# Kernel optimization log

Measured on AMD Instinct MI355X. Metric: run time of the kernel, lower is better.

The kernel has to match this reference:

```python
import jax, jax.numpy as jnp
import numpy as np

B, S, H = 2, 2048, 2048
NH, NKV, HD = 16, 8, 128
EPS = 1e-6
THETA = 10000.0
SCALE = HD ** -0.5


def setup_inputs() -> dict:
    key = jax.random.key(0)
    ks = jax.random.split(key, 6)
    return {
        "positions": jnp.tile(jnp.arange(S, dtype=jnp.int64 if jax.config.jax_enable_x64 else jnp.int32), (B, 1)),
        "hidden_states": jax.random.normal(ks[0], (B, S, H), jnp.float32),
        "residual": jax.random.normal(ks[1], (B, S, H), jnp.float32),
        "layernorm_weight": 1.0 + 0.02 * jax.random.normal(ks[2], (H,), jnp.float32),
        "qkv_weight": 0.02 * jax.random.normal(ks[3], ((NH + 2 * NKV) * HD, H), jnp.float32),
        "o_weight": 0.02 * jax.random.normal(ks[4], (H, NH * HD), jnp.float32),
        "q_norm_weight": 1.0 + 0.02 * jax.random.normal(ks[5], (HD,), jnp.float32),
        "k_norm_weight": jnp.ones((HD,), jnp.float32),
    }


def _rmsnorm(x, w, eps=EPS):
    return x * jax.lax.rsqrt(jnp.mean(x * x, axis=-1, keepdims=True) + eps) * w


def _rope(x, positions):
    # x: [B, S, h, HD]; neox-style rotate-half RoPE
    inv_freq = 1.0 / (THETA ** (jnp.arange(0, HD, 2, dtype=jnp.float32) / HD))
    ang = positions.astype(jnp.float32)[..., None] * inv_freq  # [B, S, HD/2]
    cos = jnp.cos(ang)[:, :, None, :]
    sin = jnp.sin(ang)[:, :, None, :]
    x1, x2 = jnp.split(x, 2, axis=-1)
    return jnp.concatenate([x1 * cos - x2 * sin, x2 * cos + x1 * sin], axis=-1)


def reference(positions, hidden_states, residual, layernorm_weight,
              qkv_weight, o_weight, q_norm_weight, k_norm_weight):
    # Fused RMSNorm + QKV projection (on unnormalized hidden_states)
    xn = _rmsnorm(hidden_states, layernorm_weight)
    qkv = jnp.einsum('bsh,oh->bso', xn, qkv_weight)  # [B, S, (NH+2*NKV)*HD]
    q, k, v = jnp.split(qkv, [NH * HD, (NH + NKV) * HD], axis=-1)
    q = q.reshape(B, S, NH, HD)
    k = k.reshape(B, S, NKV, HD)
    v = v.reshape(B, S, NKV, HD)
    # per-head q/k RMSNorm (q_norm in fused QKV kernel, k_norm inside attention)
    q = _rmsnorm(q, q_norm_weight)
    k = _rmsnorm(k, k_norm_weight)
    # RoPE
    q = _rope(q, positions)
    k = _rope(k, positions)
    # GQA: expand KV heads
    rep = NH // NKV
    k = jnp.repeat(k, rep, axis=2)
    v = jnp.repeat(v, rep, axis=2)
    # causal attention
    scores = jnp.einsum('bqhd,bkhd->bhqk', q, k) * SCALE
    causal = jnp.tril(jnp.ones((S, S), bool))
    scores = jnp.where(causal[None, None], scores, jnp.finfo(scores.dtype).min)
    probs = jax.nn.softmax(scores, axis=-1)
    attn = jnp.einsum('bhqk,bkhd->bqhd', probs, v).reshape(B, S, NH * HD)
    # fused output projection + residual add
    return jnp.einsum('bsd,hd->bsh', attn, o_weight) + residual
```

## Files before the change

### kernel.cpp

```cpp
#include <hip/hip_runtime.h>
#include <hip/hip_bf16.h>

typedef __attribute__((ext_vector_type(8))) short bf16x8;
typedef __attribute__((ext_vector_type(4))) float f32x4;

#define B_ 2
#define S_ 2048
#define H_ 2048
#define NH_ 16
#define NKV_ 8
#define HD_ 128
#define M_ (B_ * S_)
#define NQKV_ ((NH_ + 2 * NKV_) * HD_)
#define QK_SCALE 0.08838834764831845f

#define VMCNT(n) asm volatile("s_waitcnt vmcnt(" #n ")" ::: "memory")

__device__ __forceinline__ unsigned short f2bf(float f) {
  unsigned int u = __float_as_uint(f);
  u += 0x7fffu + ((u >> 16) & 1u);
  return (unsigned short)(u >> 16);
}
__device__ __forceinline__ float bf2f(unsigned short h) {
  return __uint_as_float(((unsigned int)h) << 16);
}
__device__ __forceinline__ void gload_lds16(const void* g, void* l) {
  __builtin_amdgcn_global_load_lds(
      (const __attribute__((address_space(1))) void*)g,
      (__attribute__((address_space(3))) void*)l, 16, 0, 0);
}

__global__ __launch_bounds__(256) void k_rmsnorm(
    const float* __restrict__ x, const float* __restrict__ w,
    unsigned short* __restrict__ out) {
  __shared__ float red[4];
  const int m = blockIdx.x;
  const int t = threadIdx.x;
  const float4* row = (const float4*)(x + (size_t)m * H_);
  float4 v0 = row[t];
  float4 v1 = row[t + 256];
  float ss = v0.x * v0.x + v0.y * v0.y + v0.z * v0.z + v0.w * v0.w +
             v1.x * v1.x + v1.y * v1.y + v1.z * v1.z + v1.w * v1.w;
#pragma unroll
  for (int mk = 1; mk < 64; mk <<= 1) ss += __shfl_xor(ss, mk);
  if ((t & 63) == 0) red[t >> 6] = ss;
  __syncthreads();
  ss = red[0] + red[1] + red[2] + red[3];
  const float sc = rsqrtf(ss * (1.0f / H_) + 1e-6f);
  const float4* wv = (const float4*)w;
  float4 w0 = wv[t], w1 = wv[t + 256];
  ushort4 o0, o1;
  o0.x = f2bf(v0.x * sc * w0.x);
  o0.y = f2bf(v0.y * sc * w0.y);
  o0.z = f2bf(v0.z * sc * w0.z);
  o0.w = f2bf(v0.w * sc * w0.w);
  o1.x = f2bf(v1.x * sc * w1.x);
  o1.y = f2bf(v1.y * sc * w1.y);
  o1.z = f2bf(v1.z * sc * w1.z);
  o1.w = f2bf(v1.w * sc * w1.w);
  ushort4* orow = (ushort4*)(out + (size_t)m * H_);
  orow[t] = o0;
  orow[t + 256] = o1;
}

__global__ __launch_bounds__(256) void k_f32_to_bf16(
    const float* __restrict__ in, unsigned short* __restrict__ out, int n4) {
  int idx = blockIdx.x * 256 + threadIdx.x;
  const int stride = gridDim.x * 256;
  for (; idx < n4; idx += stride) {
    float4 v = ((const float4*)in)[idx];
    ushort4 o;
    o.x = f2bf(v.x);
    o.y = f2bf(v.y);
    o.z = f2bf(v.z);
    o.w = f2bf(v.w);
    ((ushort4*)out)[idx] = o;
  }
}

__global__ __launch_bounds__(256) void k_rope_table(
    const int* __restrict__ positions, float* __restrict__ cos_t,
    float* __restrict__ sin_t) {
  int idx = blockIdx.x * 256 + threadIdx.x;
  if (idx >= B_ * S_ * 64) return;
  int d = idx & 63;
  int bs = idx >> 6;
  float pos = (float)positions[bs];
  float inv_freq = powf(10000.0f, -(float)(2 * d) * (1.0f / HD_));
  float ang = pos * inv_freq;
  cos_t[idx] = cosf(ang);
  sin_t[idx] = sinf(ang);
}

template <int FMB>
__device__ __forceinline__ void load_a256(const unsigned short* sAb, int wm,
                                          int lr, int lg, bf16x8 (&af)[2][4]) {
#pragma unroll
  for (int kk = 0; kk < 2; ++kk) {
    const int pc = kk * 4 + lg;
#pragma unroll
    for (int i = 0; i < 4; ++i) {
      const int R = wm + (FMB + i) * 16 + lr;
      const int idx = ((R >> 6) & 1) * 8192 +
                      ((((R >> 7) << 6) | (R & 63)) << 6) +
                      ((pc ^ (R & 7)) << 3);
      af[kk][i] = *(const bf16x8*)&sAb[idx];
    }
  }
}
template <int FNB>
__device__ __forceinline__ void load_b256(const unsigned short* sBb, int wn,
                                          int lr, int lg, bf16x8 (&bfv)[2][2]) {
#pragma unroll
  for (int kk = 0; kk < 2; ++kk) {
    const int pc = kk * 4 + lg;
#pragma unroll
    for (int j = 0; j < 2; ++j) {
      const int R = wn + (FNB + j) * 16 + lr;
      const int idx = ((R >> 5) & 1) * 8192 +
                      ((((R >> 6) << 5) | (R & 31)) << 6) +
                      ((pc ^ (R & 7)) << 3);
      bfv[kk][j] = *(const bf16x8*)&sBb[idx];
    }
  }
}

template <int FMB, int FNB>
__device__ __forceinline__ void phase_mfma(const bf16x8 (&af)[2][4],
                                           const bf16x8 (&bfv)[2][2],
                                           f32x4 (&acc)[8][4]) {
#pragma unroll
  for (int kk = 0; kk < 2; ++kk)
#pragma unroll
    for (int i = 0; i < 4; ++i)
#pragma unroll
      for (int j = 0; j < 2; ++j)
        acc[FMB + i][FNB + j] = __builtin_amdgcn_mfma_f32_16x16x32_bf16(
            af[kk][i], bfv[kk][j], acc[FMB + i][FNB + j], 0, 0, 0);
}

__global__ __launch_bounds__(512, 2) void k_gemm256(
    const unsigned short* __restrict__ A, const unsigned short* __restrict__ Bt,
    unsigned short* __restrict__ C, int M, int N, int K) {
  __shared__ unsigned short sA[2][256 * 64];
  __shared__ unsigned short sB[2][256 * 64];
  const int tid = threadIdx.x;
  const int w = tid >> 6;
  const int l = tid & 63;
  const int lr = l & 15, lg = l >> 4;
  const int gx = gridDim.x;
  const int lin = blockIdx.y * gx + blockIdx.x;
  const int cpx = (gx * gridDim.y) >> 3;
  const int swz = (lin & 7) * cpx + (lin >> 3);
  const int m0 = (swz / gx) * 256, n0 = (swz % gx) * 256;
  const int wm = (w >> 2) * 128, wn = (w & 3) * 64;
  f32x4 acc[8][4] = {};

  auto stageA = [&](int t, int bufi, int h) {
    const int k0 = t * 64;
#pragma unroll
    for (int i = 0; i < 2; ++i) {
      const int L = i * 512 + tid;
      const int r = L >> 3;
      const int R = ((r >> 6) << 7) | (h << 6) | (r & 63);
      const int d = (L & 7) ^ (r & 7);
      gload_lds16(A + (size_t)(m0 + R) * K + k0 + d * 8,
                  (char*)sA[bufi] + h * 16384 +
                      (size_t)(i * 512 + w * 64) * 16);
    }
  };
  auto stageB = [&](int t, int bufi, int h) {
    const int k0 = t * 64;
#pragma unroll
    for (int i = 0; i < 2; ++i) {
      const int L = i * 512 + tid;
      const int r = L >> 3;
      const int R = ((r >> 5) << 6) | (h << 5) | (r & 31);
      const int d = (L & 7) ^ (r & 7);
      gload_lds16(Bt + (size_t)(n0 + R) * K + k0 + d * 8,
                  (char*)sB[bufi] + h * 16384 +
                      (size_t)(i * 512 + w * 64) * 16);
    }
  };

#define BARR()                          \
  __builtin_amdgcn_s_barrier();         \
  __builtin_amdgcn_sched_barrier(0)
#define LGKM0()                                        \
  asm volatile("s_waitcnt lgkmcnt(0)" ::: "memory");   \
  __builtin_amdgcn_sched_barrier(0)

  stageA(0, 0, 0);
  stageB(0, 0, 0);
  stageB(0, 0, 1);
  stageA(0, 0, 1);
  VMCNT(2);
  BARR();

  bf16x8 af[2][4];
  bf16x8 bfv0[2][2];
  bf16x8 bfv1[2][2];
  const int NT = K >> 6;
  for (int t = 0; t < NT; ++t) {
    const int bufi = t & 1;
    const int nb = bufi ^ 1;
    const bool st = (t + 1 < NT);
    load_a256<0>(sA[bufi], wm, lr, lg, af);
    load_b256<0>(sB[bufi], wn, lr, lg, bfv0);
    load_b256<2>(sB[bufi], wn, lr, lg, bfv1);
    if (st) {
      stageA(t + 1, nb, 0);
      stageB(t + 1, nb, 0);
    }
    __builtin_amdgcn_s_barrier();
    LGKM0();
    __builtin_amdgcn_s_setprio(1);
    phase_mfma<0, 0>(af, bfv0, acc);
    phase_mfma<0, 2>(af, bfv1, acc);
    __builtin_amdgcn_s_setprio(0);
    if (st) {
      VMCNT(4);
    } else {
      VMCNT(0);
    }
    BARR();
    load_a256<4>(sA[bufi], wm, lr, lg, af);
    if (st) {
      stageB(t + 1, nb, 1);
      stageA(t + 1, nb, 1);
    }
    __builtin_amdgcn_s_barrier();
    LGKM0();
    __builtin_amdgcn_s_setprio(1);
    phase_mfma<4, 2>(af, bfv1, acc);
    phase_mfma<4, 0>(af, bfv0, acc);
    __builtin_amdgcn_s_setprio(0);
    if (st) VMCNT(2);
    BARR();
  }

#pragma unroll
  for (int fm = 0; fm < 8; ++fm)
#pragma unroll
    for (int fn = 0; fn < 4; ++fn)
#pragma unroll
      for (int r = 0; r < 4; ++r) {
        const int row = m0 + wm + fm * 16 + lg * 4 + r;
        const int col = n0 + wn + fn * 16 + lr;
        C[(size_t)row * N + col] = f2bf(acc[fm][fn][r]);
      }
#undef BARR
#undef LGKM0
}

template <int FMB>
__device__ __forceinline__ void load_ao(const unsigned short* sAb, int wm,
                                        int lr, int lg, bf16x8 (&af)[2][2]) {
#pragma unroll
  for (int kk = 0; kk < 2; ++kk) {
    const int pc = kk * 4 + lg;
#pragma unroll
    for (int i = 0; i < 2; ++i) {
      const int R = wm + (FMB + i) * 16 + lr;
      const int idx = ((R >> 5) & 1) * 8192 +
                      ((((R >> 6) << 5) | (R & 31)) << 6) +
                      ((pc ^ (R & 7)) << 3);
      af[kk][i] = *(const bf16x8*)&sAb[idx];
    }
  }
}
template <int FNB>
__device__ __forceinline__ void load_bo(const unsigned short* sBb, int wn,
                                        int lr, int lg, bf16x8 (&bfv)[2][2]) {
#pragma unroll
  for (int kk = 0; kk < 2; ++kk) {
    const int pc = kk * 4 + lg;
#pragma unroll
    for (int j = 0; j < 2; ++j) {
      const int R = wn + (FNB + j) * 16 + lr;
      const int idx = ((R >> 5) & 1) * 4096 +
                      ((((R >> 6) << 5) | (R & 31)) << 6) +
                      ((pc ^ (R & 7)) << 3);
      bfv[kk][j] = *(const bf16x8*)&sBb[idx];
    }
  }
}

template <int FMB, int FNB>
__device__ __forceinline__ void phase_mfma_o(const bf16x8 (&af)[2][2],
                                             const bf16x8 (&bfv)[2][2],
                                             f32x4 (&acc)[4][4]) {
#pragma unroll
  for (int kk = 0; kk < 2; ++kk)
#pragma unroll
    for (int i = 0; i < 2; ++i)
#pragma unroll
      for (int j = 0; j < 2; ++j)
        acc[FMB + i][FNB + j] = __builtin_amdgcn_mfma_f32_16x16x32_bf16(
            af[kk][i], bfv[kk][j], acc[FMB + i][FNB + j], 0, 0, 0);
}

__global__ __launch_bounds__(512, 1) void k_gemm_ores(
    const unsigned short* __restrict__ A, const unsigned short* __restrict__ Bt,
    float* __restrict__ Cout, const float* __restrict__ resid, int M, int N,
    int K) {
  __shared__ unsigned short sA[2][256 * 64];
  __shared__ unsigned short sB[2][128 * 64];
  const int tid = threadIdx.x;
  const int w = tid >> 6;
  const int l = tid & 63;
  const int lr = l & 15, lg = l >> 4;
  const int gx = gridDim.x;
  const int lin = blockIdx.y * gx + blockIdx.x;
  const int cpx = (gx * gridDim.y) >> 3;
  const int swz = (lin & 7) * cpx + (lin >> 3);
  const int m0 = (swz / gx) * 256, n0 = (swz % gx) * 128;
  const int wm = (w >> 1) * 64, wn = (w & 1) * 64;
  f32x4 acc[4][4] = {};

  auto stageAo = [&](int t, int bufi, int h) {
    const int k0 = t * 64;
#pragma unroll
    for (int i = 0; i < 2; ++i) {
      const int L = i * 512 + tid;
      const int r = L >> 3;
      const int R = ((r >> 5) << 6) | (h << 5) | (r & 31);
      const int d = (L & 7) ^ (r & 7);
      gload_lds16(A + (size_t)(m0 + R) * K + k0 + d * 8,
                  (char*)sA[bufi] + h * 16384 +
                      (size_t)(i * 512 + w * 64) * 16);
    }
  };
  auto stageBo = [&](int t, int bufi, int h) {
    const int k0 = t * 64;
    const int L = tid;
    const int r = L >> 3;
    const int R = ((r >> 5) << 6) | (h << 5) | (r & 31);
    const int d = (L & 7) ^ (r & 7);
    gload_lds16(Bt + (size_t)(n0 + R) * K + k0 + d * 8,
                (char*)sB[bufi] + h * 8192 + (size_t)(w * 64) * 16);
  };

#define BARR()                          \
  __builtin_amdgcn_s_barrier();         \
  __builtin_amdgcn_sched_barrier(0)
#define LGKM0()                                        \
  asm volatile("s_waitcnt lgkmcnt(0)" ::: "memory");   \
  __builtin_amdgcn_sched_barrier(0)

  stageAo(0, 0, 0);
  stageBo(0, 0, 0);
  stageBo(0, 0, 1);
  stageAo(0, 0, 1);
  VMCNT(2);
  BARR();

  bf16x8 af[2][2];
  bf16x8 bfv0[2][2];
  bf16x8 bfv1[2][2];
  const int NT = K >> 6;
  for (int t = 0; t < NT; ++t) {
    const int bufi = t & 1;
    const int nb = bufi ^ 1;
    const bool st = (t + 1 < NT);
    load_ao<0>(sA[bufi], wm, lr, lg, af);
    load_bo<0>(sB[bufi], wn, lr, lg, bfv0);
    load_bo<2>(sB[bufi], wn, lr, lg, bfv1);
    if (st) {
      stageAo(t + 1, nb, 0);
      stageBo(t + 1, nb, 0);
    }
    __builtin_amdgcn_s_barrier();
    LGKM0();
    __builtin_amdgcn_s_setprio(1);
    phase_mfma_o<0, 0>(af, bfv0, acc);
    phase_mfma_o<0, 2>(af, bfv1, acc);
    __builtin_amdgcn_s_setprio(0);
    if (st) {
      VMCNT(3);
    } else {
      VMCNT(0);
    }
    BARR();
    load_ao<2>(sA[bufi], wm, lr, lg, af);
    if (st) {
      stageBo(t + 1, nb, 1);
      stageAo(t + 1, nb, 1);
    }
    __builtin_amdgcn_s_barrier();
    LGKM0();
    __builtin_amdgcn_s_setprio(1);
    phase_mfma_o<2, 2>(af, bfv1, acc);
    phase_mfma_o<2, 0>(af, bfv0, acc);
    __builtin_amdgcn_s_setprio(0);
    if (st) VMCNT(2);
    BARR();
  }

#pragma unroll
  for (int i = 0; i < 4; ++i)
#pragma unroll
    for (int j = 0; j < 4; ++j)
#pragma unroll
      for (int r = 0; r < 4; ++r) {
        const int row = m0 + wm + i * 16 + lg * 4 + r;
        const int col = n0 + wn + j * 16 + lr;
        const size_t o = (size_t)row * N + col;
        Cout[o] = acc[i][j][r] + resid[o];
      }
#undef BARR
#undef LGKM0
}

__global__ __launch_bounds__(256) void k_postprocess(
    const unsigned short* __restrict__ qkv, const float* __restrict__ qw,
    const float* __restrict__ kw, const float* __restrict__ cos_t,
    const float* __restrict__ sin_t, unsigned short* __restrict__ qb,
    unsigned short* __restrict__ kb, unsigned short* __restrict__ vb) {
  const int m = blockIdx.x;
  const int b = m >> 11, s = m & (S_ - 1);
  const int w = threadIdx.x >> 6, l = threadIdx.x & 63;
  const unsigned short* row = qkv + (size_t)m * NQKV_;
  const float c = cos_t[(size_t)m * 64 + l];
  const float sn = sin_t[(size_t)m * 64 + l];
  for (int hh = w * 8; hh < w * 8 + 8; ++hh) {
    int base, type;
    unsigned short* out;
    const float* nw;
    if (hh < NH_) {
      type = 0;
      base = hh * HD_;
      out = qb + ((size_t)(b * NH_ + hh) * S_ + s) * HD_;
      nw = qw;
    } else if (hh < NH_ + NKV_) {
      int kh = hh - NH_;
      type = 1;
      base = NH_ * HD_ + kh * HD_;
      out = kb + ((size_t)(b * NKV_ + kh) * S_ + s) * HD_;
      nw = kw;
    } else {
      int kh = hh - NH_ - NKV_;
      type = 2;
      base = (NH_ + NKV_) * HD_ + kh * HD_;
      out = vb + ((size_t)(b * NKV_ + kh) * S_ + s) * HD_;
      nw = nullptr;
    }
    unsigned short r1 = row[base + l];
    unsigned short r2 = row[base + 64 + l];
    if (type == 2) {
      out[l] = r1;
      out[64 + l] = r2;
      continue;
    }
    float x1 = bf2f(r1), x2 = bf2f(r2);
    float ss = x1 * x1 + x2 * x2;
#pragma unroll
    for (int mk = 1; mk < 64; mk <<= 1) ss += __shfl_xor(ss, mk);
    float sc = rsqrtf(ss * (1.0f / HD_) + 1e-6f);
    float y1 = x1 * sc * nw[l];
    float y2 = x2 * sc * nw[64 + l];
    float o1 = y1 * c - y2 * sn;
    float o2 = y2 * c + y1 * sn;
    if (type == 0) {
      o1 *= QK_SCALE;
      o2 *= QK_SCALE;
    }
    out[l] = f2bf(o1);
    out[64 + l] = f2bf(o2);
  }
}

__global__ __launch_bounds__(256) void k_transpose_v(
    const unsigned short* __restrict__ in,
    unsigned short* __restrict__ out) {
  __shared__ unsigned short tile[32][33];
  const int bx = blockIdx.x, by = blockIdx.y, bz = blockIdx.z;
  const unsigned short* src = in + (size_t)bz * S_ * HD_;
  unsigned short* dst = out + (size_t)bz * S_ * HD_;
  const int tx = threadIdx.x & 31, ty = threadIdx.x >> 5;
#pragma unroll
  for (int i = ty; i < 32; i += 8)
    tile[i][tx] = src[(size_t)(bx * 32 + i) * HD_ + by * 32 + tx];
  __syncthreads();
#pragma unroll
  for (int i = ty; i < 32; i += 8)
    dst[(size_t)(by * 32 + i) * S_ + bx * 32 + tx] = tile[tx][i];
}

#define MFIX 13.0f
__global__ __launch_bounds__(512, 4) void k_attn(
    const unsigned short* __restrict__ Q,
    const unsigned short* __restrict__ K,
    const unsigned short* __restrict__ VT,
    unsigned short* __restrict__ Oa) {
  __shared__ unsigned short kt[2][64 * 128];
  __shared__ unsigned short vt[2][128 * 64];
  __shared__ unsigned short pls[8 * 16 * 64];
  const int bh = blockIdx.y;
  const int b = bh >> 4, h = bh & 15;
  const int kvh = b * NKV_ + (h >> 1);
  const int xa = blockIdx.x;
  const int xb = 31 - xa;
  const int tid = threadIdx.x;
  const int w = tid >> 6, l = tid & 63;
  const int lr = l & 15, lg = l >> 4;
  const int wr = (w & 3) * 16;
  const int myx = (w < 4) ? xa : xb;
  const int q0m = myx * 64;

  bf16x8 qf[4];
  {
    const unsigned short* Qp = Q + ((size_t)bh * S_ + q0m + wr) * HD_;
#pragma unroll
    for (int tt = 0; tt < 4; ++tt)
      qf[tt] = *(const bf16x8*)(Qp + (size_t)lr * HD_ + tt * 32 + lg * 8);
  }
  f32x4 ao[8] = {};
  float lsum = 0.f;
  const unsigned short* Kp = K + (size_t)kvh * S_ * HD_;
  const unsigned short* Vp = VT + (size_t)kvh * HD_ * S_;
  unsigned short* pw = pls + w * 1024;
  const int psw = (lr & 7) << 1;

  auto stage = [&](int t, int bufi) {
    const int k0 = t * 64;
#pragma unroll
    for (int i = 0; i < 2; ++i) {
      const int chunk = i * 512 + tid;
      {
        const int r = chunk >> 4, p = chunk & 15;
        const int d = p ^ (r & 7);
        gload_lds16(Kp + (size_t)(k0 + r) * HD_ + d * 8,
                    (char*)kt[bufi] + (size_t)(i * 512 + w * 64) * 16);
      }
      {
        const int r = chunk >> 3, p = chunk & 7;
        const int d = p ^ (r & 7);
        gload_lds16(Vp + (size_t)r * S_ + k0 + d * 8,
                    (char*)vt[bufi] + (size_t)(i * 512 + w * 64) * 16);
      }
    }
  };

  auto process = [&](int t, int bufi, bool diag) {
    const unsigned short* ktb = kt[bufi];
    const unsigned short* vtb = vt[bufi];
    f32x4 sc[4] = {};
    __builtin_amdgcn_s_setprio(1);
#pragma unroll
    for (int j = 0; j < 4; ++j)
#pragma unroll
      for (int tt = 0; tt < 4; ++tt) {
        bf16x8 kf = *(const bf16x8*)&ktb[(j * 16 + lr) * 128 +
                                         (((tt * 4 + lg) ^ (lr & 7)) << 3)];
        sc[j] =
            __builtin_amdgcn_mfma_f32_16x16x32_bf16(kf, qf[tt], sc[j], 0, 0, 0);
      }
    __builtin_amdgcn_s_setprio(0);
    if (diag) {
      const int qg = q0m + wr + lr;
      const int kvb = t * 64 + lg * 4;
#pragma unroll
      for (int j = 0; j < 4; ++j)
#pragma unroll
        for (int r = 0; r < 4; ++r)
          if (kvb + j * 16 + r > qg) sc[j][r] = -1e30f;
    }
#pragma unroll
    for (int j = 0; j < 4; ++j) {
      float p0 = __expf(sc[j][0] - MFIX);
      float p1 = __expf(sc[j][1] - MFIX);
      float p2 = __expf(sc[j][2] - MFIX);
      float p3 = __expf(sc[j][3] - MFIX);
      lsum += (p0 + p1) + (p2 + p3);
      unsigned int d0 = (unsigned int)f2bf(p0) | ((unsigned int)f2bf(p1) << 16);
      unsigned int d1 = (unsigned int)f2bf(p2) | ((unsigned int)f2bf(p3) << 16);
      const int g = (4 * j + lg) ^ psw;
      uint2 v;
      v.x = d0;
      v.y = d1;
      *(uint2*)&pw[lr * 64 + g * 4] = v;
    }
    __builtin_amdgcn_s_setprio(1);
#pragma unroll
    for (int ks = 0; ks < 2; ++ks) {
      const int g0 = (8 * ks + 2 * lg) ^ psw;
      bf16x8 pf = *(const bf16x8*)&pw[lr * 64 + g0 * 4];
#pragma unroll
      for (int dj = 0; dj < 8; ++dj) {
        bf16x8 vf = *(const bf16x8*)&vtb[(dj * 16 + lr) * 64 +
                                         (((ks * 4 + lg) ^ (lr & 7)) << 3)];
        ao[dj] =
            __builtin_amdgcn_mfma_f32_16x16x32_bf16(vf, pf, ao[dj], 0, 0, 0);
      }
    }
    __builtin_amdgcn_s_setprio(0);
  };

  stage(0, 0);
  __syncthreads();
  int cur = 0;
  for (int t = 0; t <= xb; ++t) {
    if (t < xb) stage(t + 1, cur ^ 1);
    if (t <= myx) process(t, cur, t == myx);
    __syncthreads();
    cur ^= 1;
  }

  lsum += __shfl_xor(lsum, 16);
  lsum += __shfl_xor(lsum, 32);
  const float inv = 1.0f / lsum;
  const int sg = q0m + wr + lr;
  unsigned short* orow = Oa + ((size_t)b * S_ + sg) * (NH_ * HD_) + h * HD_;
#pragma unroll
  for (int dj = 0; dj < 8; ++dj) {
    ushort4 ov;
    ov.x = f2bf(ao[dj][0] * inv);
    ov.y = f2bf(ao[dj][1] * inv);
    ov.z = f2bf(ao[dj][2] * inv);
    ov.w = f2bf(ao[dj][3] * inv);
    *(ushort4*)&orow[dj * 16 + lg * 4] = ov;
  }
}

extern "C" void kernel_launch(void* const* d_in, const int* in_sizes, int n_in,
                              void* d_out, int out_size, void* d_ws,
                              size_t ws_size, hipStream_t stream) {
  const int* positions = (const int*)d_in[0];
  const float* hidden = (const float*)d_in[1];
  const float* residual = (const float*)d_in[2];
  const float* ln_w = (const float*)d_in[3];
  const float* qkv_w = (const float*)d_in[4];
  const float* o_w = (const float*)d_in[5];
  const float* q_nw = (const float*)d_in[6];
  const float* k_nw = (const float*)d_in[7];

  char* ws = (char*)d_ws;
  const size_t SZ_XN = (size_t)M_ * H_ * 2;
  const size_t SZ_QKVW = (size_t)NQKV_ * H_ * 2;
  const size_t SZ_OW = (size_t)H_ * (NH_ * HD_) * 2;
  const size_t SZ_QKV = (size_t)M_ * NQKV_ * 2;
  const size_t SZ_KB = (size_t)B_ * NKV_ * S_ * HD_ * 2;
  const size_t SZ_COS = (size_t)B_ * S_ * 64 * 4;

  unsigned short* xn = (unsigned short*)(ws);
  unsigned short* q_buf = (unsigned short*)(ws);
  unsigned short* qkvw_bf = (unsigned short*)(ws + SZ_XN);
  unsigned short* k_buf = (unsigned short*)(ws + SZ_XN);
  unsigned short* v_buf = (unsigned short*)(ws + SZ_XN + SZ_KB);
  unsigned short* owbf = (unsigned short*)(ws + SZ_XN + SZ_QKVW);
  unsigned short* qkv_bf = (unsigned short*)(ws + SZ_XN + SZ_QKVW + SZ_OW);
  unsigned short* attn_o = qkv_bf;
  unsigned short* vt_buf =
      (unsigned short*)(ws + SZ_XN + SZ_QKVW + SZ_OW + SZ_QKV);
  float* cos_t = (float*)(ws + SZ_XN + SZ_QKVW + SZ_OW + SZ_QKV + SZ_KB);
  float* sin_t = (float*)((char*)cos_t + SZ_COS);

  k_rmsnorm<<<M_, 256, 0, stream>>>(hidden, ln_w, xn);
  k_f32_to_bf16<<<2048, 256, 0, stream>>>(qkv_w, qkvw_bf,
                                          (int)(SZ_QKVW / 2 / 4));
  k_f32_to_bf16<<<1024, 256, 0, stream>>>(o_w, owbf, (int)(SZ_OW / 2 / 4));
  k_rope_table<<<(B_ * S_ * 64) / 256, 256, 0, stream>>>(positions, cos_t,
                                                         sin_t);
  k_gemm256<<<dim3(NQKV_ / 256, M_ / 256), 512, 0, stream>>>(
      xn, qkvw_bf, qkv_bf, M_, NQKV_, H_);
  k_postprocess<<<M_, 256, 0, stream>>>(qkv_bf, q_nw, k_nw, cos_t, sin_t,
                                        q_buf, k_buf, v_buf);
  k_transpose_v<<<dim3(S_ / 32, HD_ / 32, B_ * NKV_), 256, 0, stream>>>(v_buf,
                                                                        vt_buf);
  k_attn<<<dim3(16, B_ * NH_), 512, 0, stream>>>(q_buf, k_buf, vt_buf, attn_o);
  k_gemm_ores<<<dim3((NH_ * HD_) / 128, M_ / 256), 512, 0, stream>>>(
      attn_o, owbf, (float*)d_out, residual, M_, NH_ * HD_, H_);
}
```

Baseline: 222.4 us.

## Rebalance causal attention work by splitting late KV tiles between wave groups

In the paired-tile causal attention kernel, group A waves used to finish their short query tile early and then idle while group B processed the long tile. Now group A writes its output early, reloads Q for tile B, and takes half of each remaining KV tile (score columns 32-63). Group B handles the other half (columns 0-31). The partial accumulators and row sums are merged through LDS at the end, with a fixed-max softmax so the merge is a plain sum. This adds register pressure, an extra Q reload and an LDS reduction, and leaves the per-tile MFMA work split unevenly.

```diff
diff --git a/kernel.cpp b/kernel.cpp
--- a/kernel.cpp
+++ b/kernel.cpp
@@ -488,6 +488,71 @@
 }
 
 #define MFIX 13.0f
+
+template <int PART>
+__device__ __forceinline__ void attn_proc(
+    const unsigned short* __restrict__ ktb,
+    const unsigned short* __restrict__ vtb, const bf16x8 (&qf)[4],
+    f32x4 (&ao)[8], float& lsum, unsigned short* __restrict__ pw, int lr,
+    int lg, int psw, int qg, int kvb0, bool diag) {
+  constexpr int J0 = (PART == 2) ? 2 : 0;
+  constexpr int J1 = (PART == 1) ? 2 : 4;
+  constexpr int KS0 = (PART == 2) ? 1 : 0;
+  constexpr int KS1 = (PART == 1) ? 1 : 2;
+  f32x4 sc[4];
+  __builtin_amdgcn_s_setprio(1);
+#pragma unroll
+  for (int j = J0; j < J1; ++j) {
+    sc[j][0] = 0.f;
+    sc[j][1] = 0.f;
+    sc[j][2] = 0.f;
+    sc[j][3] = 0.f;
+#pragma unroll
+    for (int tt = 0; tt < 4; ++tt) {
+      bf16x8 kf = *(const bf16x8*)&ktb[(j * 16 + lr) * 128 +
+                                       (((tt * 4 + lg) ^ (lr & 7)) << 3)];
+      sc[j] =
+          __builtin_amdgcn_mfma_f32_16x16x32_bf16(kf, qf[tt], sc[j], 0, 0, 0);
+    }
+  }
+  __builtin_amdgcn_s_setprio(0);
+  if (diag) {
+#pragma unroll
+    for (int j = J0; j < J1; ++j)
+#pragma unroll
+      for (int r = 0; r < 4; ++r)
+        if (kvb0 + j * 16 + r > qg) sc[j][r] = -1e30f;
+  }
+#pragma unroll
+  for (int j = J0; j < J1; ++j) {
+    float p0 = __expf(sc[j][0] - MFIX);
+    float p1 = __expf(sc[j][1] - MFIX);
+    float p2 = __expf(sc[j][2] - MFIX);
+    float p3 = __expf(sc[j][3] - MFIX);
+    lsum += (p0 + p1) + (p2 + p3);
+    unsigned int d0 = (unsigned int)f2bf(p0) | ((unsigned int)f2bf(p1) << 16);
+    unsigned int d1 = (unsigned int)f2bf(p2) | ((unsigned int)f2bf(p3) << 16);
+    const int g = (4 * j + lg) ^ psw;
+    uint2 v;
+    v.x = d0;
+    v.y = d1;
+    *(uint2*)&pw[lr * 64 + g * 4] = v;
+  }
+  __builtin_amdgcn_s_setprio(1);
+#pragma unroll
+  for (int ks = KS0; ks < KS1; ++ks) {
+    const int g0 = (8 * ks + 2 * lg) ^ psw;
+    bf16x8 pf = *(const bf16x8*)&pw[lr * 64 + g0 * 4];
+#pragma unroll
+    for (int dj = 0; dj < 8; ++dj) {
+      bf16x8 vf = *(const bf16x8*)&vtb[(dj * 16 + lr) * 64 +
+                                       (((ks * 4 + lg) ^ (lr & 7)) << 3)];
+      ao[dj] = __builtin_amdgcn_mfma_f32_16x16x32_bf16(vf, pf, ao[dj], 0, 0, 0);
+    }
+  }
+  __builtin_amdgcn_s_setprio(0);
+}
+
 __global__ __launch_bounds__(512, 4) void k_attn(
     const unsigned short* __restrict__ Q,
     const unsigned short* __restrict__ K,
@@ -504,13 +569,14 @@
   const int tid = threadIdx.x;
   const int w = tid >> 6, l = tid & 63;
   const int lr = l & 15, lg = l >> 4;
-  const int wr = (w & 3) * 16;
-  const int myx = (w < 4) ? xa : xb;
-  const int q0m = myx * 64;
+  const int band = (w & 3) * 16;
+  const bool isA = (w < 4);
+  const int q0a = xa * 64, q0b = xb * 64;
 
   bf16x8 qf[4];
   {
-    const unsigned short* Qp = Q + ((size_t)bh * S_ + q0m + wr) * HD_;
+    const int qr = (isA ? q0a : q0b) + band;
+    const unsigned short* Qp = Q + ((size_t)bh * S_ + qr) * HD_;
 #pragma unroll
     for (int tt = 0; tt < 4; ++tt)
       qf[tt] = *(const bf16x8*)(Qp + (size_t)lr * HD_ + tt * 32 + lg * 8);
@@ -542,84 +608,95 @@
     }
   };
 
-  auto process = [&](int t, int bufi, bool diag) {
-    const unsigned short* ktb = kt[bufi];
-    const unsigned short* vtb = vt[bufi];
-    f32x4 sc[4] = {};
-    __builtin_amdgcn_s_setprio(1);
-#pragma unroll
-    for (int j = 0; j < 4; ++j)
-#pragma unroll
-      for (int tt = 0; tt < 4; ++tt) {
-        bf16x8 kf = *(const bf16x8*)&ktb[(j * 16 + lr) * 128 +
-                                         (((tt * 4 + lg) ^ (lr & 7)) << 3)];
-        sc[j] =
-            __builtin_amdgcn_mfma_f32_16x16x32_bf16(kf, qf[tt], sc[j], 0, 0, 0);
-      }
-    __builtin_amdgcn_s_setprio(0);
-    if (diag) {
-      const int qg = q0m + wr + lr;
-      const int kvb = t * 64 + lg * 4;
-#pragma unroll
-      for (int j = 0; j < 4; ++j)
-#pragma unroll
-        for (int r = 0; r < 4; ++r)
-          if (kvb + j * 16 + r > qg) sc[j][r] = -1e30f;
-    }
-#pragma unroll
-    for (int j = 0; j < 4; ++j) {
-      float p0 = __expf(sc[j][0] - MFIX);
-      float p1 = __expf(sc[j][1] - MFIX);
-      float p2 = __expf(sc[j][2] - MFIX);
-      float p3 = __expf(sc[j][3] - MFIX);
-      lsum += (p0 + p1) + (p2 + p3);
-      unsigned int d0 = (unsigned int)f2bf(p0) | ((unsigned int)f2bf(p1) << 16);
-      unsigned int d1 = (unsigned int)f2bf(p2) | ((unsigned int)f2bf(p3) << 16);
-      const int g = (4 * j + lg) ^ psw;
-      uint2 v;
-      v.x = d0;
-      v.y = d1;
-      *(uint2*)&pw[lr * 64 + g * 4] = v;
-    }
-    __builtin_amdgcn_s_setprio(1);
-#pragma unroll
-    for (int ks = 0; ks < 2; ++ks) {
-      const int g0 = (8 * ks + 2 * lg) ^ psw;
-      bf16x8 pf = *(const bf16x8*)&pw[lr * 64 + g0 * 4];
-#pragma unroll
-      for (int dj = 0; dj < 8; ++dj) {
-        bf16x8 vf = *(const bf16x8*)&vtb[(dj * 16 + lr) * 64 +
-                                         (((ks * 4 + lg) ^ (lr & 7)) << 3)];
-        ao[dj] =
-            __builtin_amdgcn_mfma_f32_16x16x32_bf16(vf, pf, ao[dj], 0, 0, 0);
-      }
-    }
-    __builtin_amdgcn_s_setprio(0);
-  };
-
   stage(0, 0);
   __syncthreads();
   int cur = 0;
   for (int t = 0; t <= xb; ++t) {
     if (t < xb) stage(t + 1, cur ^ 1);
-    if (t <= myx) process(t, cur, t == myx);
+    if (isA) {
+      if (t <= xa) {
+        attn_proc<0>(kt[cur], vt[cur], qf, ao, lsum, pw, lr, lg, psw,
+                     q0a + band + lr, t * 64 + lg * 4, t == xa);
+      } else {
+        if (t == xa + 1) {
+          float ls = lsum;
+          ls += __shfl_xor(ls, 16);
+          ls += __shfl_xor(ls, 32);
+          const float inv = 1.0f / ls;
+          const int sg = q0a + band + lr;
+          unsigned short* orow =
+              Oa + ((size_t)b * S_ + sg) * (NH_ * HD_) + h * HD_;
+#pragma unroll
+          for (int dj = 0; dj < 8; ++dj) {
+            ushort4 ov;
+            ov.x = f2bf(ao[dj][0] * inv);
+            ov.y = f2bf(ao[dj][1] * inv);
+            ov.z = f2bf(ao[dj][2] * inv);
+            ov.w = f2bf(ao[dj][3] * inv);
+            *(ushort4*)&orow[dj * 16 + lg * 4] = ov;
+          }
+#pragma unroll
+          for (int dj = 0; dj < 8; ++dj) {
+            ao[dj][0] = 0.f;
+            ao[dj][1] = 0.f;
+            ao[dj][2] = 0.f;
+            ao[dj][3] = 0.f;
+          }
+          lsum = 0.f;
+          const unsigned short* Qp = Q + ((size_t)bh * S_ + q0b + band) * HD_;
+#pragma unroll
+          for (int tt = 0; tt < 4; ++tt)
+            qf[tt] =
+                *(const bf16x8*)(Qp + (size_t)lr * HD_ + tt * 32 + lg * 8);
+        }
+        attn_proc<2>(kt[cur], vt[cur], qf, ao, lsum, pw, lr, lg, psw,
+                     q0b + band + lr, t * 64 + lg * 4, t == xb);
+      }
+    } else {
+      if (t <= xa)
+        attn_proc<0>(kt[cur], vt[cur], qf, ao, lsum, pw, lr, lg, psw,
+                     q0b + band + lr, t * 64 + lg * 4, false);
+      else
+        attn_proc<1>(kt[cur], vt[cur], qf, ao, lsum, pw, lr, lg, psw,
+                     q0b + band + lr, t * 64 + lg * 4, t == xb);
+    }
     __syncthreads();
     cur ^= 1;
   }
 
-  lsum += __shfl_xor(lsum, 16);
-  lsum += __shfl_xor(lsum, 32);
-  const float inv = 1.0f / lsum;
-  const int sg = q0m + wr + lr;
-  unsigned short* orow = Oa + ((size_t)b * S_ + sg) * (NH_ * HD_) + h * HD_;
-#pragma unroll
-  for (int dj = 0; dj < 8; ++dj) {
-    ushort4 ov;
-    ov.x = f2bf(ao[dj][0] * inv);
-    ov.y = f2bf(ao[dj][1] * inv);
-    ov.z = f2bf(ao[dj][2] * inv);
-    ov.w = f2bf(ao[dj][3] * inv);
-    *(ushort4*)&orow[dj * 16 + lg * 4] = ov;
+  float ls = lsum;
+  ls += __shfl_xor(ls, 16);
+  ls += __shfl_xor(ls, 32);
+  float* exp_ao = (float*)kt;
+  float* exp_ls = (float*)vt;
+  if (isA) {
+#pragma unroll
+    for (int dj = 0; dj < 8; ++dj)
+#pragma unroll
+      for (int r = 0; r < 4; ++r)
+        exp_ao[(dj * 4 + r) * 256 + (w & 3) * 64 + l] = ao[dj][r];
+    if (lg == 0) exp_ls[(w & 3) * 16 + lr] = ls;
+  }
+  __syncthreads();
+  if (!isA) {
+#pragma unroll
+    for (int dj = 0; dj < 8; ++dj)
+#pragma unroll
+      for (int r = 0; r < 4; ++r)
+        ao[dj][r] += exp_ao[(dj * 4 + r) * 256 + (w & 3) * 64 + l];
+    ls += exp_ls[(w & 3) * 16 + lr];
+    const float inv = 1.0f / ls;
+    const int sg = q0b + band + lr;
+    unsigned short* orow = Oa + ((size_t)b * S_ + sg) * (NH_ * HD_) + h * HD_;
+#pragma unroll
+    for (int dj = 0; dj < 8; ++dj) {
+      ushort4 ov;
+      ov.x = f2bf(ao[dj][0] * inv);
+      ov.y = f2bf(ao[dj][1] * inv);
+      ov.z = f2bf(ao[dj][2] * inv);
+      ov.w = f2bf(ao[dj][3] * inv);
+      *(ushort4*)&orow[dj * 16 + lg * 4] = ov;
+    }
   }
 }
 
```

Result: no change. 226.2 us (+1.7%).
